# Kernel optimization log

Measured on AMD Instinct MI355X. Metric: run time of the kernel, lower is better.

The kernel has to match this reference:

```python
import jax, jax.numpy as jnp
import numpy as np
from math import sqrt


def setup_inputs() -> dict:
    key = jax.random.key(0)
    kq, kk, kv = jax.random.split(key, 3)
    B, L, H, E = 4, 2048, 8, 64
    S, D = L, E
    return {
        "queries": jax.random.normal(kq, (B, L, H, E), dtype=jnp.float32),
        "keys": jax.random.normal(kk, (B, S, H, E), dtype=jnp.float32),
        "values": jax.random.normal(kv, (B, S, H, D), dtype=jnp.float32),
    }


def reference(queries, keys, values):
    # FullAttention with mask_flag=True (TriangularCausalMask), dropout p=0,
    # output_attention=False. scale = 1/sqrt(E).
    B, L, H, E = queries.shape
    S = keys.shape[1]
    scale = 1.0 / sqrt(E)
    # scores: [B, H, L, S]
    scores = jnp.einsum("blhe,bshe->bhls", queries, keys)
    # causal mask: positions s > l are masked (upper triangle above diagonal)
    causal = jnp.tril(jnp.ones((L, S), dtype=bool))  # True = keep
    neg_inf = jnp.finfo(scores.dtype).min
    scores = jnp.where(causal, scores, neg_inf)
    A = jax.nn.softmax(scale * scores, axis=-1)  # [B,H,L,S]
    # context: [B, L, H, D]
    V = jnp.einsum("bhls,bshd->blhd", A, values)
    return V
```

## Files before the change

kernel.cpp:

```cpp
#include <hip/hip_runtime.h>
#include <math.h>

#define BD 4
#define LD 2048
#define HD 8
#define ED 64
#define TQ 64
#define TK 64
#define RS (HD * ED)
#define NT 32
#define TILE_BYTES 8192

typedef __attribute__((ext_vector_type(8))) _Float16 f16x8;
typedef __attribute__((ext_vector_type(4))) _Float16 f16x4;
typedef __attribute__((ext_vector_type(4))) float f32x4;
typedef __attribute__((ext_vector_type(4))) unsigned int u32x4;
typedef __attribute__((ext_vector_type(2))) unsigned int u32x2;
typedef unsigned int u32;
typedef unsigned long long u64;

__device__ inline u32 pkh(float a, float b) {
    return __builtin_bit_cast(u32, __builtin_amdgcn_cvt_pkrtz(a, b));
}
__device__ inline u64 pkh4(float a, float b, float c, float d) {
    return (u64)pkh(a, b) | ((u64)pkh(c, d) << 32);
}
__device__ inline int swz(int row, int bcol) {
    return row * 128 + ((((bcol >> 4) ^ row) & 7) << 4) + (bcol & 15);
}
__device__ __forceinline__ void gload_lds16(const char* g, char* l) {
    __builtin_amdgcn_global_load_lds(
        (const __attribute__((address_space(1))) unsigned int*)g,
        (__attribute__((address_space(3))) unsigned int*)l, 16, 0, 0);
}

__global__ __launch_bounds__(256, 4)
void cvt_kv(const float* __restrict__ K, const float* __restrict__ V,
            char* __restrict__ Kimg, char* __restrict__ Vimg) {
    const int t  = threadIdx.x;
    const int b  = blockIdx.x >> 3;
    const int h  = blockIdx.x & 7;
    const int kt = blockIdx.y;

    const int ks  = t >> 2;
    const int ke0 = (t & 3) << 2;
    const int vs0 = (t & 15) << 2;
    const int vd0 = (t >> 4) << 2;

    const size_t tb = ((size_t)((b * HD + h) * NT + kt)) * TILE_BYTES;
    char* kd = Kimg + tb;
    char* vd = Vimg + tb;

    const float* kp = K + ((size_t)((b * LD + kt * TK + ks) * HD + h)) * ED + ke0;
    const float* vp = V + ((size_t)((b * LD + kt * TK + vs0) * HD + h)) * ED + vd0;

    float4 kx[4], vx[4];
    #pragma unroll
    for (int j = 0; j < 4; ++j) kx[j] = *(const float4*)(kp + 16 * j);
    #pragma unroll
    for (int r = 0; r < 4; ++r) vx[r] = *(const float4*)(vp + r * RS);

    #pragma unroll
    for (int j = 0; j < 4; ++j)
        *(u64*)(kd + swz(ks, 2 * (ke0 + 16 * j))) = pkh4(kx[j].x, kx[j].y, kx[j].z, kx[j].w);
    *(u64*)(vd + swz(vd0 + 0, 2 * vs0)) = pkh4(vx[0].x, vx[1].x, vx[2].x, vx[3].x);
    *(u64*)(vd + swz(vd0 + 1, 2 * vs0)) = pkh4(vx[0].y, vx[1].y, vx[2].y, vx[3].y);
    *(u64*)(vd + swz(vd0 + 2, 2 * vs0)) = pkh4(vx[0].z, vx[1].z, vx[2].z, vx[3].z);
    *(u64*)(vd + swz(vd0 + 3, 2 * vs0)) = pkh4(vx[0].w, vx[1].w, vx[2].w, vx[3].w);
}

__global__ __launch_bounds__(256, 4)
void fa_f16img(const char* __restrict__ Kimg, const char* __restrict__ Vimg,
               const float* __restrict__ Q, float* __restrict__ O) {
    __shared__ __align__(16) char smem[32768];

    const int t    = threadIdx.x;
    const int lane = t & 63;
    const int w    = t >> 6;
    const int m16  = lane & 15;
    const int quad = lane >> 4;

    const int b = blockIdx.x >> 3;
    const int h = blockIdx.x & 7;
    const int y  = (int)blockIdx.y;
    const int r  = y & 7;
    const int c  = y >> 3;
    const int qt = (c == 0) ? (31 - r) : (c == 1) ? (r + 8)
                 : (c == 2) ? (23 - r) : r;
    const int q0  = qt * TQ;
    const int len = qt + 1;

    const char* Kt = Kimg + (size_t)(b * HD + h) * NT * TILE_BYTES;
    const char* Vt = Vimg + (size_t)(b * HD + h) * NT * TILE_BYTES;
    const int lsrc = (w << 10) + (lane << 4);
    const int ldst = (w << 10);

    const float qscale = 0.125f * 1.44269504088896340736f;
    f16x8 qf[2];
    {
        const float* qrow =
            Q + ((size_t)((b * LD + q0 + (w << 4) + m16) * HD + h)) * ED;
        #pragma unroll
        for (int hf = 0; hf < 2; ++hf) {
            const float4 x  = *(const float4*)(qrow + hf * 32 + quad * 8);
            const float4 y4 = *(const float4*)(qrow + hf * 32 + quad * 8 + 4);
            u32x4 p;
            p[0] = pkh(x.x * qscale, x.y * qscale);
            p[1] = pkh(x.z * qscale, x.w * qscale);
            p[2] = pkh(y4.x * qscale, y4.y * qscale);
            p[3] = pkh(y4.z * qscale, y4.w * qscale);
            qf[hf] = __builtin_bit_cast(f16x8, p);
        }
    }

    f32x4 oacc[4];
    float l_i = 0.0f;
    #pragma unroll
    for (int nt = 0; nt < 4; ++nt) oacc[nt] = (f32x4){0.f, 0.f, 0.f, 0.f};

    {
        const char* ks = Kt;
        const char* vs = Vt;
        #pragma unroll
        for (int inst = 0; inst < 2; ++inst) {
            gload_lds16(ks + inst * 4096 + lsrc, smem + inst * 4096 + ldst);
            gload_lds16(vs + inst * 4096 + lsrc, smem + 16384 + inst * 4096 + ldst);
        }
    }
    __syncthreads();

    for (int kt = 0; kt < len; ++kt) {
        char* rK = smem + ((kt & 1) << 13);
        char* rV = smem + 16384 + ((kt & 1) << 13);

        if (kt < len - 1) {
            const char* ks = Kt + (size_t)(kt + 1) * TILE_BYTES;
            const char* vs = Vt + (size_t)(kt + 1) * TILE_BYTES;
            const int bo = ((kt & 1) ^ 1) << 13;
            #pragma unroll
            for (int inst = 0; inst < 2; ++inst) {
                gload_lds16(ks + inst * 4096 + lsrc, smem + bo + inst * 4096 + ldst);
                gload_lds16(vs + inst * 4096 + lsrc, smem + 16384 + bo + inst * 4096 + ldst);
            }
        }

        f32x4 sacc[4];
        #pragma unroll
        for (int kc = 0; kc < 4; ++kc) {
            const f16x8 kf0 = *(const f16x8*)(rK + swz(kc * 16 + m16, quad * 16));
            const f16x8 kf1 = *(const f16x8*)(rK + swz(kc * 16 + m16, 64 + quad * 16));
            f32x4 z = {0.f, 0.f, 0.f, 0.f};
            z = __builtin_amdgcn_mfma_f32_16x16x32_f16(kf0, qf[0], z, 0, 0, 0);
            z = __builtin_amdgcn_mfma_f32_16x16x32_f16(kf1, qf[1], z, 0, 0, 0);
            sacc[kc] = z;
        }

        if (kt == qt) {
            const int ql = (w << 4) + m16;
            #pragma unroll
            for (int kc = 0; kc < 4; ++kc)
                #pragma unroll
                for (int i = 0; i < 4; ++i)
                    if (kc * 16 + quad * 4 + i > ql) sacc[kc][i] = -INFINITY;
        }

        f16x4 pf[4];
        #pragma unroll
        for (int kc = 0; kc < 4; ++kc) {
            float p0 = __builtin_amdgcn_exp2f(sacc[kc][0]);
            float p1 = __builtin_amdgcn_exp2f(sacc[kc][1]);
            float p2 = __builtin_amdgcn_exp2f(sacc[kc][2]);
            float p3 = __builtin_amdgcn_exp2f(sacc[kc][3]);
            l_i += (p0 + p1) + (p2 + p3);
            u32x2 pp;
            pp[0] = pkh(p0, p1);
            pp[1] = pkh(p2, p3);
            pf[kc] = __builtin_bit_cast(f16x4, pp);
        }

        #pragma unroll
        for (int kc = 0; kc < 4; ++kc) {
            #pragma unroll
            for (int dt = 0; dt < 4; ++dt) {
                const f16x4 vf = *(const f16x4*)
                    (rV + swz(dt * 16 + m16, 2 * (kc * 16 + quad * 4)));
                oacc[dt] = __builtin_amdgcn_mfma_f32_16x16x16f16(vf, pf[kc], oacc[dt], 0, 0, 0);
            }
        }

        __syncthreads();
    }

    {
        float l = l_i;
        l += __shfl_xor(l, 16);
        l += __shfl_xor(l, 32);
        const float inv = 1.0f / l;
        float* orow =
            O + ((size_t)((b * LD + q0 + (w << 4) + m16) * HD + h)) * ED;
        #pragma unroll
        for (int dt = 0; dt < 4; ++dt) {
            float4 o;
            o.x = oacc[dt][0] * inv;
            o.y = oacc[dt][1] * inv;
            o.z = oacc[dt][2] * inv;
            o.w = oacc[dt][3] * inv;
            *(float4*)(orow + dt * 16 + quad * 4) = o;
        }
    }
}

__global__ __launch_bounds__(256, 4)
void fa_mfma_q64(const float* __restrict__ Q, const float* __restrict__ K,
                 const float* __restrict__ V, float* __restrict__ O) {
    __shared__ __align__(16) char smem[32768];
    const int t = threadIdx.x, lane = t & 63, w = t >> 6;
    const int m16 = lane & 15, quad = lane >> 4;
    const int b = blockIdx.x >> 3, h = blockIdx.x & 7;
    const int y = (int)blockIdx.y, r = y & 7, c = y >> 3;
    const int qt = (c == 0) ? (31 - r) : (c == 1) ? (r + 8) : (c == 2) ? (23 - r) : r;
    const int q0 = qt * TQ;
    const int len = qt + 1;
    const int ks = t >> 2, ke0 = (t & 3) << 2;
    const int vs0 = (t & 15) << 2, vd0 = (t >> 4) << 2;
    const float* Kbase = K + ((size_t)((b * LD + ks) * HD + h)) * ED + ke0;
    const float* Vbase = V + ((size_t)((b * LD + vs0) * HD + h)) * ED + vd0;
    const float qscale = 0.125f * 1.44269504088896340736f;
    f16x8 qf[2];
    {
        const float* qrow = Q + ((size_t)((b * LD + q0 + (w << 4) + m16) * HD + h)) * ED;
        #pragma unroll
        for (int hf = 0; hf < 2; ++hf) {
            const float4 x = *(const float4*)(qrow + hf * 32 + quad * 8);
            const float4 y4 = *(const float4*)(qrow + hf * 32 + quad * 8 + 4);
            u32x4 p;
            p[0] = pkh(x.x * qscale, x.y * qscale);
            p[1] = pkh(x.z * qscale, x.w * qscale);
            p[2] = pkh(y4.x * qscale, y4.y * qscale);
            p[3] = pkh(y4.z * qscale, y4.w * qscale);
            qf[hf] = __builtin_bit_cast(f16x8, p);
        }
    }
    f32x4 oacc[4];
    float l_i = 0.0f;
    #pragma unroll
    for (int nt = 0; nt < 4; ++nt) oacc[nt] = (f32x4){0.f, 0.f, 0.f, 0.f};
    float4 kx[4], vx[4];
    {
        #pragma unroll
        for (int j = 0; j < 4; ++j) kx[j] = *(const float4*)(Kbase + 16 * j);
        #pragma unroll
        for (int rr = 0; rr < 4; ++rr) vx[rr] = *(const float4*)(Vbase + rr * RS);
        char* wK = smem;
        char* wV = smem + 16384;
        #pragma unroll
        for (int j = 0; j < 4; ++j)
            *(u64*)(wK + swz(ks, 2 * (ke0 + 16 * j))) = pkh4(kx[j].x, kx[j].y, kx[j].z, kx[j].w);
        *(u64*)(wV + swz(vd0 + 0, 2 * vs0)) = pkh4(vx[0].x, vx[1].x, vx[2].x, vx[3].x);
        *(u64*)(wV + swz(vd0 + 1, 2 * vs0)) = pkh4(vx[0].y, vx[1].y, vx[2].y, vx[3].y);
        *(u64*)(wV + swz(vd0 + 2, 2 * vs0)) = pkh4(vx[0].z, vx[1].z, vx[2].z, vx[3].z);
        *(u64*)(wV + swz(vd0 + 3, 2 * vs0)) = pkh4(vx[0].w, vx[1].w, vx[2].w, vx[3].w);
    }
    __syncthreads();
    for (int kt = 0; kt < len; ++kt) {
        char* rK = smem + ((kt & 1) << 13);
        char* rV = smem + 16384 + ((kt & 1) << 13);
        const bool pre = kt < len - 1;
        if (pre) {
            const float* kp = Kbase + (size_t)(kt + 1) * (TK * RS);
            const float* vp = Vbase + (size_t)(kt + 1) * (TK * RS);
            #pragma unroll
            for (int j = 0; j < 4; ++j) kx[j] = *(const float4*)(kp + 16 * j);
            #pragma unroll
            for (int rr = 0; rr < 4; ++rr) vx[rr] = *(const float4*)(vp + rr * RS);
        }
        f32x4 sacc[4];
        #pragma unroll
        for (int kc = 0; kc < 4; ++kc) {
            const f16x8 kf0 = *(const f16x8*)(rK + swz(kc * 16 + m16, quad * 16));
            const f16x8 kf1 = *(const f16x8*)(rK + swz(kc * 16 + m16, 64 + quad * 16));
            f32x4 z = {0.f, 0.f, 0.f, 0.f};
            z = __builtin_amdgcn_mfma_f32_16x16x32_f16(kf0, qf[0], z, 0, 0, 0);
            z = __builtin_amdgcn_mfma_f32_16x16x32_f16(kf1, qf[1], z, 0, 0, 0);
            sacc[kc] = z;
        }
        if (kt == qt) {
            const int ql = (w << 4) + m16;
            #pragma unroll
            for (int kc = 0; kc < 4; ++kc)
                #pragma unroll
                for (int i = 0; i < 4; ++i)
                    if (kc * 16 + quad * 4 + i > ql) sacc[kc][i] = -INFINITY;
        }
        f16x4 pf[4];
        #pragma unroll
        for (int kc = 0; kc < 4; ++kc) {
            float p0 = __builtin_amdgcn_exp2f(sacc[kc][0]);
            float p1 = __builtin_amdgcn_exp2f(sacc[kc][1]);
            float p2 = __builtin_amdgcn_exp2f(sacc[kc][2]);
            float p3 = __builtin_amdgcn_exp2f(sacc[kc][3]);
            l_i += (p0 + p1) + (p2 + p3);
            u32x2 pp;
            pp[0] = pkh(p0, p1);
            pp[1] = pkh(p2, p3);
            pf[kc] = __builtin_bit_cast(f16x4, pp);
        }
        #pragma unroll
        for (int kc = 0; kc < 4; ++kc) {
            #pragma unroll
            for (int dt = 0; dt < 4; ++dt) {
                const f16x4 vf = *(const f16x4*)
                    (rV + swz(dt * 16 + m16, 2 * (kc * 16 + quad * 4)));
                oacc[dt] = __builtin_amdgcn_mfma_f32_16x16x16f16(vf, pf[kc], oacc[dt], 0, 0, 0);
            }
        }
        if (pre) {
            char* wK = smem + ((kt & 1) ? 0 : 8192);
            char* wV = smem + 16384 + ((kt & 1) ? 0 : 8192);
            #pragma unroll
            for (int j = 0; j < 4; ++j)
                *(u64*)(wK + swz(ks, 2 * (ke0 + 16 * j))) = pkh4(kx[j].x, kx[j].y, kx[j].z, kx[j].w);
            *(u64*)(wV + swz(vd0 + 0, 2 * vs0)) = pkh4(vx[0].x, vx[1].x, vx[2].x, vx[3].x);
            *(u64*)(wV + swz(vd0 + 1, 2 * vs0)) = pkh4(vx[0].y, vx[1].y, vx[2].y, vx[3].y);
            *(u64*)(wV + swz(vd0 + 2, 2 * vs0)) = pkh4(vx[0].z, vx[1].z, vx[2].z, vx[3].z);
            *(u64*)(wV + swz(vd0 + 3, 2 * vs0)) = pkh4(vx[0].w, vx[1].w, vx[2].w, vx[3].w);
        }
        __syncthreads();
    }
    {
        float l = l_i;
        l += __shfl_xor(l, 16);
        l += __shfl_xor(l, 32);
        const float inv = 1.0f / l;
        float* orow = O + ((size_t)((b * LD + q0 + (w << 4) + m16) * HD + h)) * ED;
        #pragma unroll
        for (int dt = 0; dt < 4; ++dt) {
            float4 o;
            o.x = oacc[dt][0] * inv;
            o.y = oacc[dt][1] * inv;
            o.z = oacc[dt][2] * inv;
            o.w = oacc[dt][3] * inv;
            *(float4*)(orow + dt * 16 + quad * 4) = o;
        }
    }
}

extern "C" void kernel_launch(void* const* d_in, const int* in_sizes, int n_in,
                              void* d_out, int out_size, void* d_ws, size_t ws_size,
                              hipStream_t stream) {
    const float* Q = (const float*)d_in[0];
    const float* K = (const float*)d_in[1];
    const float* V = (const float*)d_in[2];
    float* O = (float*)d_out;

    const size_t img = (size_t)BD * HD * NT * TILE_BYTES;
    if (d_ws != nullptr && ws_size >= 2 * img) {
        char* Kimg = (char*)d_ws;
        char* Vimg = (char*)d_ws + img;
        cvt_kv<<<dim3(BD * HD, NT), 256, 0, stream>>>(K, V, Kimg, Vimg);
        fa_f16img<<<dim3(BD * HD, 32), 256, 0, stream>>>(Kimg, Vimg, Q, O);
    } else {
        fa_mfma_q64<<<dim3(BD * HD, 32), 256, 0, stream>>>(Q, K, V, O);
    }
}
```

Baseline: 120.0 us.

## Split key dimension across waves and reduce partial outputs through LDS

Each wave now covers all 64 query rows of the tile and handles only its own 16-key slice of each K/V tile, rather than owning 16 query rows across all 64 keys. K and V fragments are loaded once per wave per tile and reused across four query sub-blocks, which cuts LDS reads per tile. Partial output accumulators and row sums are combined across waves through LDS in a multi-step reduction before wave 0 normalizes and writes. In exchange, accumulator registers grow fourfold and occupancy drops to 3 blocks per SM. The reduction adds extra LDS traffic and barriers, and the first K/V tile is now prefetched before Q is loaded.

```diff
diff --git a/kernel.cpp b/kernel.cpp
--- a/kernel.cpp
+++ b/kernel.cpp
@@ -69,10 +69,10 @@
     *(u64*)(vd + swz(vd0 + 3, 2 * vs0)) = pkh4(vx[0].w, vx[1].w, vx[2].w, vx[3].w);
 }
 
-__global__ __launch_bounds__(256, 4)
+__global__ __launch_bounds__(256, 3)
 void fa_f16img(const char* __restrict__ Kimg, const char* __restrict__ Vimg,
                const float* __restrict__ Q, float* __restrict__ O) {
-    __shared__ __align__(16) char smem[32768];
+    __shared__ __align__(16) char smem[33792];
 
     const int t    = threadIdx.x;
     const int lane = t & 63;
@@ -95,11 +95,18 @@
     const int lsrc = (w << 10) + (lane << 4);
     const int ldst = (w << 10);
 
+    #pragma unroll
+    for (int inst = 0; inst < 2; ++inst) {
+        gload_lds16(Kt + inst * 4096 + lsrc, smem + inst * 4096 + ldst);
+        gload_lds16(Vt + inst * 4096 + lsrc, smem + 16384 + inst * 4096 + ldst);
+    }
+
     const float qscale = 0.125f * 1.44269504088896340736f;
-    f16x8 qf[2];
-    {
+    f16x8 qf[4][2];
+    #pragma unroll
+    for (int qs = 0; qs < 4; ++qs) {
         const float* qrow =
-            Q + ((size_t)((b * LD + q0 + (w << 4) + m16) * HD + h)) * ED;
+            Q + ((size_t)((b * LD + q0 + (qs << 4) + m16) * HD + h)) * ED;
         #pragma unroll
         for (int hf = 0; hf < 2; ++hf) {
             const float4 x  = *(const float4*)(qrow + hf * 32 + quad * 8);
@@ -109,24 +116,24 @@
             p[1] = pkh(x.z * qscale, x.w * qscale);
             p[2] = pkh(y4.x * qscale, y4.y * qscale);
             p[3] = pkh(y4.z * qscale, y4.w * qscale);
-            qf[hf] = __builtin_bit_cast(f16x8, p);
-        }
-    }
-
-    f32x4 oacc[4];
-    float l_i = 0.0f;
-    #pragma unroll
-    for (int nt = 0; nt < 4; ++nt) oacc[nt] = (f32x4){0.f, 0.f, 0.f, 0.f};
-
-    {
-        const char* ks = Kt;
-        const char* vs = Vt;
-        #pragma unroll
-        for (int inst = 0; inst < 2; ++inst) {
-            gload_lds16(ks + inst * 4096 + lsrc, smem + inst * 4096 + ldst);
-            gload_lds16(vs + inst * 4096 + lsrc, smem + 16384 + inst * 4096 + ldst);
-        }
-    }
+            qf[qs][hf] = __builtin_bit_cast(f16x8, p);
+        }
+    }
+
+    f32x4 oacc[4][4];
+    float l_i[4] = {0.f, 0.f, 0.f, 0.f};
+    #pragma unroll
+    for (int dt = 0; dt < 4; ++dt)
+        #pragma unroll
+        for (int qs = 0; qs < 4; ++qs) oacc[dt][qs] = (f32x4){0.f, 0.f, 0.f, 0.f};
+
+    const int swK0 = swz((w << 4) + m16, quad * 16);
+    const int swK1 = swz((w << 4) + m16, 64 + quad * 16);
+    int swV[4];
+    #pragma unroll
+    for (int dt = 0; dt < 4; ++dt)
+        swV[dt] = swz(dt * 16 + m16, (w << 5) + (quad << 3));
+
     __syncthreads();
 
     for (int kt = 0; kt < len; ++kt) {
@@ -134,78 +141,121 @@
         char* rV = smem + 16384 + ((kt & 1) << 13);
 
         if (kt < len - 1) {
-            const char* ks = Kt + (size_t)(kt + 1) * TILE_BYTES;
-            const char* vs = Vt + (size_t)(kt + 1) * TILE_BYTES;
+            const char* ksrc = Kt + (size_t)(kt + 1) * TILE_BYTES;
+            const char* vsrc = Vt + (size_t)(kt + 1) * TILE_BYTES;
             const int bo = ((kt & 1) ^ 1) << 13;
             #pragma unroll
             for (int inst = 0; inst < 2; ++inst) {
-                gload_lds16(ks + inst * 4096 + lsrc, smem + bo + inst * 4096 + ldst);
-                gload_lds16(vs + inst * 4096 + lsrc, smem + 16384 + bo + inst * 4096 + ldst);
+                gload_lds16(ksrc + inst * 4096 + lsrc, smem + bo + inst * 4096 + ldst);
+                gload_lds16(vsrc + inst * 4096 + lsrc, smem + 16384 + bo + inst * 4096 + ldst);
             }
         }
 
-        f32x4 sacc[4];
-        #pragma unroll
-        for (int kc = 0; kc < 4; ++kc) {
-            const f16x8 kf0 = *(const f16x8*)(rK + swz(kc * 16 + m16, quad * 16));
-            const f16x8 kf1 = *(const f16x8*)(rK + swz(kc * 16 + m16, 64 + quad * 16));
+        const f16x8 kf0 = *(const f16x8*)(rK + swK0);
+        const f16x8 kf1 = *(const f16x8*)(rK + swK1);
+        f16x4 vf[4];
+        #pragma unroll
+        for (int dt = 0; dt < 4; ++dt)
+            vf[dt] = *(const f16x4*)(rV + swV[dt]);
+
+        const bool diag = (kt == qt);
+        #pragma unroll
+        for (int qs = 0; qs < 4; ++qs) {
             f32x4 z = {0.f, 0.f, 0.f, 0.f};
-            z = __builtin_amdgcn_mfma_f32_16x16x32_f16(kf0, qf[0], z, 0, 0, 0);
-            z = __builtin_amdgcn_mfma_f32_16x16x32_f16(kf1, qf[1], z, 0, 0, 0);
-            sacc[kc] = z;
-        }
-
-        if (kt == qt) {
-            const int ql = (w << 4) + m16;
-            #pragma unroll
-            for (int kc = 0; kc < 4; ++kc)
+            z = __builtin_amdgcn_mfma_f32_16x16x32_f16(kf0, qf[qs][0], z, 0, 0, 0);
+            z = __builtin_amdgcn_mfma_f32_16x16x32_f16(kf1, qf[qs][1], z, 0, 0, 0);
+
+            if (diag) {
+                const int ql = (qs << 4) + m16;
+                const int sl = (w << 4) + (quad << 2);
                 #pragma unroll
                 for (int i = 0; i < 4; ++i)
-                    if (kc * 16 + quad * 4 + i > ql) sacc[kc][i] = -INFINITY;
-        }
-
-        f16x4 pf[4];
-        #pragma unroll
-        for (int kc = 0; kc < 4; ++kc) {
-            float p0 = __builtin_amdgcn_exp2f(sacc[kc][0]);
-            float p1 = __builtin_amdgcn_exp2f(sacc[kc][1]);
-            float p2 = __builtin_amdgcn_exp2f(sacc[kc][2]);
-            float p3 = __builtin_amdgcn_exp2f(sacc[kc][3]);
-            l_i += (p0 + p1) + (p2 + p3);
+                    if (sl + i > ql) z[i] = -INFINITY;
+            }
+
+            float p0 = __builtin_amdgcn_exp2f(z[0]);
+            float p1 = __builtin_amdgcn_exp2f(z[1]);
+            float p2 = __builtin_amdgcn_exp2f(z[2]);
+            float p3 = __builtin_amdgcn_exp2f(z[3]);
+            l_i[qs] += (p0 + p1) + (p2 + p3);
             u32x2 pp;
             pp[0] = pkh(p0, p1);
             pp[1] = pkh(p2, p3);
-            pf[kc] = __builtin_bit_cast(f16x4, pp);
-        }
-
-        #pragma unroll
-        for (int kc = 0; kc < 4; ++kc) {
-            #pragma unroll
-            for (int dt = 0; dt < 4; ++dt) {
-                const f16x4 vf = *(const f16x4*)
-                    (rV + swz(dt * 16 + m16, 2 * (kc * 16 + quad * 4)));
-                oacc[dt] = __builtin_amdgcn_mfma_f32_16x16x16f16(vf, pf[kc], oacc[dt], 0, 0, 0);
-            }
+            const f16x4 pf = __builtin_bit_cast(f16x4, pp);
+
+            #pragma unroll
+            for (int dt = 0; dt < 4; ++dt)
+                oacc[dt][qs] = __builtin_amdgcn_mfma_f32_16x16x16f16(vf[dt], pf, oacc[dt][qs], 0, 0, 0);
         }
 
         __syncthreads();
     }
 
-    {
-        float l = l_i;
+    #pragma unroll
+    for (int qs = 0; qs < 4; ++qs) {
+        float l = l_i[qs];
         l += __shfl_xor(l, 16);
         l += __shfl_xor(l, 32);
-        const float inv = 1.0f / l;
-        float* orow =
-            O + ((size_t)((b * LD + q0 + (w << 4) + m16) * HD + h)) * ED;
-        #pragma unroll
-        for (int dt = 0; dt < 4; ++dt) {
-            float4 o;
-            o.x = oacc[dt][0] * inv;
-            o.y = oacc[dt][1] * inv;
-            o.z = oacc[dt][2] * inv;
-            o.w = oacc[dt][3] * inv;
-            *(float4*)(orow + dt * 16 + quad * 4) = o;
+        l_i[qs] = l;
+    }
+    float* lbuf = (float*)(smem + 32768);
+    if (quad == 0) {
+        #pragma unroll
+        for (int qs = 0; qs < 4; ++qs)
+            lbuf[(w << 6) + (qs << 4) + m16] = l_i[qs];
+    }
+    if (w >= 2) {
+        char* reg = smem + ((w - 2) << 14);
+        #pragma unroll
+        for (int dt = 0; dt < 4; ++dt)
+            #pragma unroll
+            for (int qs = 0; qs < 4; ++qs)
+                *(f32x4*)(reg + ((((dt << 2) | qs)) << 10) + (lane << 4)) = oacc[dt][qs];
+    }
+    __syncthreads();
+    if (w < 2) {
+        char* reg = smem + (w << 14);
+        #pragma unroll
+        for (int dt = 0; dt < 4; ++dt)
+            #pragma unroll
+            for (int qs = 0; qs < 4; ++qs)
+                oacc[dt][qs] += *(const f32x4*)(reg + ((((dt << 2) | qs)) << 10) + (lane << 4));
+    }
+    __syncthreads();
+    if (w == 1) {
+        char* reg = smem;
+        #pragma unroll
+        for (int dt = 0; dt < 4; ++dt)
+            #pragma unroll
+            for (int qs = 0; qs < 4; ++qs)
+                *(f32x4*)(reg + ((((dt << 2) | qs)) << 10) + (lane << 4)) = oacc[dt][qs];
+    }
+    __syncthreads();
+    if (w == 0) {
+        char* reg = smem;
+        float inv[4];
+        #pragma unroll
+        for (int qs = 0; qs < 4; ++qs)
+            inv[qs] = 1.0f / (lbuf[(qs << 4) + m16] + lbuf[64 + (qs << 4) + m16] +
+                              lbuf[128 + (qs << 4) + m16] + lbuf[192 + (qs << 4) + m16]);
+        #pragma unroll
+        for (int dt = 0; dt < 4; ++dt)
+            #pragma unroll
+            for (int qs = 0; qs < 4; ++qs)
+                oacc[dt][qs] += *(const f32x4*)(reg + ((((dt << 2) | qs)) << 10) + (lane << 4));
+        #pragma unroll
+        for (int qs = 0; qs < 4; ++qs) {
+            float* orow =
+                O + ((size_t)((b * LD + q0 + (qs << 4) + m16) * HD + h)) * ED;
+            #pragma unroll
+            for (int dt = 0; dt < 4; ++dt) {
+                float4 o;
+                o.x = oacc[dt][qs][0] * inv[qs];
+                o.y = oacc[dt][qs][1] * inv[qs];
+                o.z = oacc[dt][qs][2] * inv[qs];
+                o.w = oacc[dt][qs][3] * inv[qs];
+                *(float4*)(orow + dt * 16 + (quad << 2)) = o;
+            }
         }
     }
 }
```

Measured after the change: 120.7 us. About the same (+0.6%).
